# Optimization experiments

Hardware: AMD Instinct MI355X
Metric: run time of the kernel (lower is better)

The kernel has to match this reference:

```python
import jax, jax.numpy as jnp
import numpy as np

THRESHOLD = 0.2
NEG_POS_RATIO = 3
ALPHA = 1.0
B, M, P, C = 64, 50, 24564, 2


def cxcy_to_xy(c):
    return jnp.concatenate([c[..., :2] - c[..., 2:] / 2, c[..., :2] + c[..., 2:] / 2], axis=-1)


def xy_to_cxcy(x):
    return jnp.concatenate([(x[..., :2] + x[..., 2:]) / 2, x[..., 2:] - x[..., :2]], axis=-1)


def cxcy_to_gcxgcy(c, p):
    # SSD encoding: offsets scaled by 10, sizes (log) scaled by 5
    return jnp.concatenate([(c[..., :2] - p[..., :2]) / (p[..., 2:] / 10.0),
                            jnp.log(c[..., 2:] / p[..., 2:]) * 5.0], axis=-1)


def jaccard(a, b):
    # a: (M,4) xy boxes, b: (P,4) xy boxes -> (M,P) IoU
    lt = jnp.maximum(a[:, None, :2], b[None, :, :2])
    rb = jnp.minimum(a[:, None, 2:], b[None, :, 2:])
    inter = jnp.prod(jnp.clip(rb - lt, 0.0), axis=-1)
    area_a = jnp.prod(a[:, 2:] - a[:, :2], axis=-1)
    area_b = jnp.prod(b[:, 2:] - b[:, :2], axis=-1)
    return inter / (area_a[:, None] + area_b[None, :] - inter)


def setup_inputs() -> dict:
    key = jax.random.key(0)
    k1, k2, k3, k4, k5, k6 = jax.random.split(key, 6)
    predicted_locs = jax.random.normal(k1, (B, P, 4), dtype=jnp.float32)
    predicted_scores = jax.random.normal(k2, (B, P, C), dtype=jnp.float32)
    # valid GT corner boxes in [0,1]: x2>x1, y2>y1
    xy1 = jax.random.uniform(k3, (B, M, 2), minval=0.0, maxval=0.75)
    wh = jax.random.uniform(k4, (B, M, 2), minval=0.05, maxval=0.25)
    boxes = jnp.concatenate([xy1, xy1 + wh], axis=-1).astype(jnp.float32)
    # priors in cxcywh with positive sizes
    pc = jax.random.uniform(k5, (P, 2), minval=0.0, maxval=1.0)
    pwh = jax.random.uniform(k6, (P, 2), minval=0.02, maxval=0.3)
    priors_cxcy = jnp.concatenate([pc, pwh], axis=-1).astype(jnp.float32)
    return {"predicted_locs": predicted_locs, "predicted_scores": predicted_scores,
            "boxes": boxes, "priors_cxcy": priors_cxcy}


def reference(predicted_locs, predicted_scores, boxes, priors_cxcy):
    n_priors = priors_cxcy.shape[0]
    priors_xy = cxcy_to_xy(priors_cxcy)

    def assign(boxes_i):  # boxes_i: (M,4) xy
        overlap = jaccard(boxes_i, priors_xy)  # (M,P)
        overlap_for_each_prior = overlap.max(axis=0)        # (P,)
        object_for_each_prior = overlap.argmax(axis=0)      # (P,)
        prior_for_each_object = overlap.argmax(axis=1)      # (M,)
        # force each object's best prior to be assigned to that object
        object_for_each_prior = object_for_each_prior.at[prior_for_each_object].set(jnp.arange(boxes_i.shape[0]))
        overlap_for_each_prior = overlap_for_each_prior.at[prior_for_each_object].set(1.0)
        labels = jnp.where(overlap_for_each_prior < THRESHOLD, 0, 1).astype(jnp.int32)
        true_locs = cxcy_to_gcxgcy(xy_to_cxcy(boxes_i[object_for_each_prior]), priors_cxcy)
        return labels, true_locs

    true_classes, true_locs = jax.vmap(assign)(boxes)  # (B,P), (B,P,4)
    pos = true_classes != 0                            # (B,P)
    n_pos = pos.sum(axis=1)                            # (B,)
    total_pos = n_pos.sum().astype(jnp.float32)

    # L1Loss(mean) over the positive-prior coordinates
    loc_abs = jnp.abs(predicted_locs - true_locs)
    loc_loss = jnp.sum(loc_abs * pos[..., None]) / (total_pos * 4.0)

    # per-prior cross entropy
    logp = jax.nn.log_softmax(predicted_scores, axis=-1)
    conf_all = -jnp.take_along_axis(logp, true_classes[..., None].astype(jnp.int32), axis=-1)[..., 0]  # (B,P)
    conf_pos_sum = jnp.sum(conf_all * pos)

    # hard negative mining: zero positives, sort descending, take top 3*n_pos per image
    conf_neg = jnp.where(pos, 0.0, conf_all)
    conf_neg_sorted = -jnp.sort(-conf_neg, axis=1)
    ranks = jnp.arange(n_priors)[None, :]
    hard = ranks < (NEG_POS_RATIO * n_pos)[:, None]
    conf_hard_sum = jnp.sum(conf_neg_sorted * hard)

    conf_loss = (conf_hard_sum + conf_pos_sum) / total_pos
    return conf_loss + ALPHA * loc_loss
```

## Files before the change

### kernel.cpp

```cpp
#include <hip/hip_runtime.h>
#include <math.h>

#define BB 64
#define MM 50
#define PP 24564
#define NBLK 96
#define THRESH 0.2f
#define P4 (PP / 4)
#define SLACK 64u
#define NCH 24
#define WMARG 0.151f
#define RCPM 8u
#define NBINS 64
#define GBIN 8
#define BINBLK 24
#define SELCH 8
#define SCH4 ((P4 + SELCH - 1) / SELCH)
#define CAP PP

__device__ __forceinline__ float l1loc(float4 bxm, float4 pc, float4 pl) {
    float cx = (bxm.x + bxm.z) * 0.5f, cy = (bxm.y + bxm.w) * 0.5f;
    float w = bxm.z - bxm.x, h = bxm.w - bxm.y;
    float g0 = (cx - pc.x) / (pc.z * 0.1f);
    float g1 = (cy - pc.y) / (pc.w * 0.1f);
    float g2 = logf(w / pc.z) * 5.0f;
    float g3 = logf(h / pc.w) * 5.0f;
    return fabsf(pl.x - g0) + fabsf(pl.y - g1) + fabsf(pl.z - g2) + fabsf(pl.w - g3);
}

__global__ void k_init(int* __restrict__ ghist, int* __restrict__ ghist2,
                       int* __restrict__ gcur, unsigned long long* __restrict__ Lm) {
    int i = blockIdx.x * 256 + threadIdx.x;
    if (i < BB * 2048) ghist[i] = 0;
    if (i < BB * 1024) ghist2[i] = 0;
    if (i < BB) gcur[i] = 0;
    if (i < BB * MM) Lm[i] = 0x00000000FFFFFFFFull;
}

__global__ void k_bin_count(const float4* __restrict__ pr_cxcy, int* __restrict__ blkcnt) {
    __shared__ int h[NBINS];
    int tid = threadIdx.x;
    if (tid < NBINS) h[tid] = 0;
    __syncthreads();
    for (int p = blockIdx.x * 256 + tid; p < PP; p += BINBLK * 256) {
        float4 c = pr_cxcy[p];
        int bx = min(GBIN - 1, (int)(c.x * GBIN));
        int by = min(GBIN - 1, (int)(c.y * GBIN));
        atomicAdd(&h[by * GBIN + bx], 1);
    }
    __syncthreads();
    if (tid < NBINS) blkcnt[blockIdx.x * NBINS + tid] = h[tid];
}

__global__ void k_bin_scan(const int* __restrict__ blkcnt, int* __restrict__ blkbase) {
    __shared__ int s[NBINS];
    int tid = threadIdx.x;
    int cnt = 0;
    for (int k = 0; k < BINBLK; ++k) cnt += blkcnt[k * NBINS + tid];
    int v = cnt;
    s[tid] = v;
    __syncthreads();
    for (int off = 1; off < NBINS; off <<= 1) {
        int add = (tid >= off) ? s[tid - off] : 0;
        __syncthreads();
        v += add;
        s[tid] = v;
        __syncthreads();
    }
    int base = v - cnt;
    for (int k = 0; k < BINBLK; ++k) {
        blkbase[k * NBINS + tid] = base;
        base += blkcnt[k * NBINS + tid];
    }
}

__global__ void k_bin_scatter(const float4* __restrict__ pr_cxcy,
                              const int* __restrict__ blkbase,
                              float4* __restrict__ perm_pc,
                              int* __restrict__ perm_orig,
                              int* __restrict__ invperm) {
    __shared__ int cur[NBINS];
    int tid = threadIdx.x;
    if (tid < NBINS) cur[tid] = blkbase[blockIdx.x * NBINS + tid];
    __syncthreads();
    for (int p = blockIdx.x * 256 + tid; p < PP; p += BINBLK * 256) {
        float4 c = pr_cxcy[p];
        int bx = min(GBIN - 1, (int)(c.x * GBIN));
        int by = min(GBIN - 1, (int)(c.y * GBIN));
        int pos = atomicAdd(&cur[by * GBIN + bx], 1);
        perm_pc[pos] = c;
        perm_orig[pos] = p;
        invperm[p] = pos;
    }
}

__global__ void k_tilebb(const float4* __restrict__ perm_pc, float4* __restrict__ tilebox) {
    int t = blockIdx.x, tid = threadIdx.x;
    int slot = t * 256 + tid;
    float x1 = 1e30f, y1 = 1e30f, x2 = -1e30f, y2 = -1e30f;
    if (slot < PP) {
        float4 c = perm_pc[slot];
        x1 = c.x - c.z * 0.5f; y1 = c.y - c.w * 0.5f;
        x2 = c.x + c.z * 0.5f; y2 = c.y + c.w * 0.5f;
    }
    __shared__ float sx1[256], sy1[256], sx2[256], sy2[256];
    sx1[tid] = x1; sy1[tid] = y1; sx2[tid] = x2; sy2[tid] = y2;
    __syncthreads();
    for (int s = 128; s > 0; s >>= 1) {
        if (tid < s) {
            sx1[tid] = fminf(sx1[tid], sx1[tid + s]);
            sy1[tid] = fminf(sy1[tid], sy1[tid + s]);
            sx2[tid] = fmaxf(sx2[tid], sx2[tid + s]);
            sy2[tid] = fmaxf(sy2[tid], sy2[tid + s]);
        }
        __syncthreads();
    }
    if (tid == 0) tilebox[t] = make_float4(sx1[0], sy1[0], sx2[0], sy2[0]);
}

__global__ void k_main(const float4* __restrict__ boxes,
                       const float4* __restrict__ perm_pc,
                       const int* __restrict__ perm_orig,
                       const float4* __restrict__ tilebox,
                       const float4* __restrict__ plocs,
                       const float2* __restrict__ scores,
                       unsigned long long* __restrict__ Lm,
                       float* __restrict__ bestv,
                       int* __restrict__ bmv,
                       float* __restrict__ confneg,
                       int* __restrict__ ghist,
                       int* __restrict__ npos_part,
                       float* __restrict__ cpos_part,
                       float* __restrict__ loc_part) {
    int b = blockIdx.y;
    int slot = blockIdx.x * 256 + threadIdx.x;
    int tid = threadIdx.x;
    __shared__ float4 sbox[MM];
    __shared__ float sarea[MM];
    __shared__ unsigned long long smax[MM];
    __shared__ int shist[2048];
    __shared__ int si[256];
    __shared__ float s1[256], s2[256];
    __shared__ unsigned char slist[64];
    __shared__ int s_nc;
    for (int i = tid; i < 2048; i += 256) shist[i] = 0;
    if (tid < MM) {
        float4 bxt = boxes[b * MM + tid];
        sbox[tid] = bxt;
        sarea[tid] = (bxt.z - bxt.x) * (bxt.w - bxt.y);
        smax[tid] = 0ull;
    }
    __syncthreads();
    if (tid < 64) {
        float4 tb = tilebox[blockIdx.x];
        bool flag = false;
        if (tid < MM) {
            float4 bxm = sbox[tid];
            flag = !(bxm.x > tb.z || bxm.z < tb.x || bxm.y > tb.w || bxm.w < tb.y);
        }
        unsigned long long mask = __ballot(flag);
        if (flag) {
            int rank = __popcll(mask & ((1ull << tid) - 1));
            slist[rank] = (unsigned char)tid;
        }
        if (tid == 0) s_nc = __popcll(mask);
    }
    __syncthreads();

    int np = 0;
    float cpos = 0.0f, lloc = 0.0f;
    if (slot < PP) {
        float4 pc = perm_pc[slot];
        int orig = perm_orig[slot];
        float px1 = pc.x - pc.z * 0.5f, py1 = pc.y - pc.w * 0.5f;
        float px2 = pc.x + pc.z * 0.5f, py2 = pc.y + pc.w * 0.5f;
        float pa = (px2 - px1) * (py2 - py1);
        float binter = 0.0f, bdenom = 1.0f;
        int bm = 0;
        int nc = s_nc;
        for (int j = 0; j < nc; ++j) {
            int m = (int)slist[j];
            float4 bxm = sbox[m];
            float lx = fmaxf(bxm.x, px1), ly = fmaxf(bxm.y, py1);
            float rx = fminf(bxm.z, px2), ry = fminf(bxm.w, py2);
            float iw = fmaxf(rx - lx, 0.0f), ih = fmaxf(ry - ly, 0.0f);
            float inter = iw * ih;
            float den = sarea[m] + pa - inter;
            float l = inter * bdenom, r = binter * den;
            if (l > r) { binter = inter; bdenom = den; bm = m; }
        }
        float q = binter / bdenom;
        size_t sidx = (size_t)b * PP + slot;
        size_t oidx = (size_t)b * PP + orig;
        bestv[sidx] = q;
        bmv[sidx] = bm;
        unsigned long long key =
            ((unsigned long long)__float_as_uint(q) << 32) | (unsigned int)(~orig);
        atomicMax(&smax[bm], key);
        bool pos = (q >= THRESH);
        float2 sc = scores[oidx];
        float mx = fmaxf(sc.x, sc.y);
        float lse = mx + logf(expf(sc.x - mx) + expf(sc.y - mx));
        float conf = pos ? (lse - sc.y) : (lse - sc.x);
        float ck = pos ? 0.0f : conf;
        confneg[sidx] = ck;
        atomicAdd(&shist[__float_as_uint(ck) >> 20], 1);
        if (pos) {
            np = 1;
            cpos = conf;
            lloc = l1loc(sbox[bm], pc, plocs[oidx]);
        }
    }
    si[tid] = np; s1[tid] = cpos; s2[tid] = lloc;
    __syncthreads();
    for (int s = 128; s > 0; s >>= 1) {
        if (tid < s) {
            si[tid] += si[tid + s];
            s1[tid] += s1[tid + s];
            s2[tid] += s2[tid + s];
        }
        __syncthreads();
    }
    if (tid == 0) {
        int o = b * NBLK + blockIdx.x;
        npos_part[o] = si[0];
        cpos_part[o] = s1[0];
        loc_part[o] = s2[0];
    }
    if (tid < MM) {
        unsigned long long v = smax[tid];
        if (v) atomicMax(&Lm[b * MM + tid], v);
    }
    for (int i = tid; i < 2048; i += 256) {
        int c = shist[i];
        if (c) atomicAdd(&ghist[b * 2048 + i], c);
    }
}

__global__ void k_bpo3(const float4* __restrict__ boxes,
                       const float4* __restrict__ perm_pc,
                       const int* __restrict__ perm_orig,
                       const float* __restrict__ bestv,
                       unsigned long long* __restrict__ Lm) {
    int b = blockIdx.y, c = blockIdx.x, tid = threadIdx.x;
    __shared__ float4 sbox[MM];
    __shared__ float sarea[MM];
    __shared__ unsigned thr[MM];
    __shared__ unsigned thrs[MM];
    __shared__ unsigned char order[MM];
    __shared__ unsigned long long smax[MM];
    if (tid < MM) {
        float4 bxt = boxes[b * MM + tid];
        sbox[tid] = bxt;
        sarea[tid] = (bxt.z - bxt.x) * (bxt.w - bxt.y);
        unsigned long long L = Lm[b * MM + tid];
        smax[tid] = L;
        unsigned hi = (unsigned)(L >> 32);
        thr[tid] = (hi > SLACK) ? hi - SLACK : 0u;
    }
    __syncthreads();
    if (tid < MM) {
        unsigned tj = thr[tid];
        int rank = 0;
        for (int k = 0; k < MM; ++k) {
            unsigned tk = thr[k];
            if (tk < tj || (tk == tj && k < tid)) rank++;
        }
        order[rank] = (unsigned char)tid;
        thrs[rank] = tj;
    }
    __syncthreads();
    const unsigned* smax_hi = ((const unsigned*)smax) + 1;
    const float4* bv4 = (const float4*)(bestv + (size_t)b * PP);
    int i = c * 256 + tid;
    unsigned qb4[4] = {0u, 0u, 0u, 0u};
    int porig[4] = {0, 0, 0, 0};
    float4 pc4[4];
    float px1r[4], py1r[4], px2r[4], py2r[4], par[4];
    #pragma unroll
    for (int e = 0; e < 4; ++e) pc4[e] = make_float4(-10.0f, -10.0f, 0.0f, 0.0f);
    if (i < P4) {
        float4 qv = bv4[i];
        qb4[0] = __float_as_uint(qv.x); qb4[1] = __float_as_uint(qv.y);
        qb4[2] = __float_as_uint(qv.z); qb4[3] = __float_as_uint(qv.w);
        #pragma unroll
        for (int e = 0; e < 4; ++e) {
            pc4[e] = perm_pc[4 * i + e];
            porig[e] = perm_orig[4 * i + e];
        }
    }
    #pragma unroll
    for (int e = 0; e < 4; ++e) {
        px1r[e] = pc4[e].x - pc4[e].z * 0.5f;
        py1r[e] = pc4[e].y - pc4[e].w * 0.5f;
        px2r[e] = pc4[e].x + pc4[e].z * 0.5f;
        py2r[e] = pc4[e].y + pc4[e].w * 0.5f;
        par[e] = (px2r[e] - px1r[e]) * (py2r[e] - py1r[e]);
    }
    unsigned wqb = max(max(qb4[0], qb4[1]), max(qb4[2], qb4[3]));
    #pragma unroll
    for (int off = 32; off > 0; off >>= 1)
        wqb = max(wqb, (unsigned)__shfl_xor((int)wqb, off));

    unsigned thrv = thrs[0];
    int j = (int)order[0];
    float4 bxm = sbox[j];
    float am = sarea[j];
    unsigned hi = smax_hi[2 * j];
    for (int jj = 0; jj < MM; ++jj) {
        if (thrv > wqb) break;
        unsigned thrv_n = 0xFFFFFFFFu;
        int j_n = 0;
        float4 bxm_n = make_float4(0.0f, 0.0f, 0.0f, 0.0f);
        float am_n = 0.0f;
        unsigned hi_n = 0u;
        if (jj + 1 < MM) {
            thrv_n = thrs[jj + 1];
            j_n = (int)order[jj + 1];
            bxm_n = sbox[j_n];
            am_n = sarea[j_n];
            hi_n = smax_hi[2 * j_n];
        }
        unsigned long long hikey = ((unsigned long long)hi) << 32;
        #pragma unroll
        for (int e = 0; e < 4; ++e) {
            if (qb4[e] < thrv) continue;
            float4 pc = pc4[e];
            if (pc.x < bxm.x - WMARG || pc.x > bxm.z + WMARG ||
                pc.y < bxm.y - WMARG || pc.y > bxm.w + WMARG) continue;
            float lx = fmaxf(bxm.x, px1r[e]), ly = fmaxf(bxm.y, py1r[e]);
            float rx = fminf(bxm.z, px2r[e]), ry = fminf(bxm.w, py2r[e]);
            float iw = fmaxf(rx - lx, 0.0f), ih = fmaxf(ry - ly, 0.0f);
            float inter = iw * ih;
            float den = am + par[e] - inter;
            float qa = inter * __builtin_amdgcn_rcpf(den);
            if (__float_as_uint(qa) + RCPM < hi) continue;
            float q = inter / den;
            unsigned long long key =
                ((unsigned long long)__float_as_uint(q) << 32) |
                (unsigned int)(~porig[e]);
            if (key > hikey) atomicMax(&smax[j], key);
        }
        thrv = thrv_n; j = j_n; bxm = bxm_n; am = am_n; hi = hi_n;
    }
    __syncthreads();
    if (tid < MM) atomicMax(&Lm[b * MM + tid], smax[tid]);
}

__device__ __forceinline__ float block_sum(float v, float* fred, int tid) {
    fred[tid] = v;
    __syncthreads();
    for (int s = 128; s > 0; s >>= 1) {
        if (tid < s) fred[tid] += fred[tid + s];
        __syncthreads();
    }
    float r = fred[0];
    __syncthreads();
    return r;
}

template <int NB>
__device__ __forceinline__ void suffix_find(const int* __restrict__ h, int K, int tid,
                                            int* iscr, int* bcast, int slot) {
    const int c = NB / 256;
    const int base = tid * c;
    int tsum = 0;
    #pragma unroll
    for (int i = 0; i < c; ++i) tsum += h[base + i];
    iscr[tid] = tsum;
    __syncthreads();
    int val = tsum;
    for (int off = 1; off < 256; off <<= 1) {
        int other = (tid + off < 256) ? iscr[tid + off] : 0;
        __syncthreads();
        val += other;
        iscr[tid] = val;
        __syncthreads();
    }
    int acc = val - tsum;
    int best = -1, cg = 0;
    for (int i = base + c - 1; i >= base; --i) {
        int s = acc + h[i];
        if (s >= K) { best = i; cg = acc; break; }
        acc = s;
    }
    iscr[tid] = best;
    __syncthreads();
    for (int s2 = 128; s2 > 0; s2 >>= 1) {
        if (tid < s2) iscr[tid] = max(iscr[tid], iscr[tid + s2]);
        __syncthreads();
    }
    int gbest = iscr[0];
    __syncthreads();
    if (best == gbest && best >= 0) { bcast[slot] = gbest; bcast[slot + 1] = cg; }
    __syncthreads();
}

__global__ void k_selKF(const float4* __restrict__ boxes,
                        const float4* __restrict__ pr_cxcy,
                        const float4* __restrict__ plocs,
                        const float2* __restrict__ scores,
                        const unsigned long long* __restrict__ Lm,
                        const int* __restrict__ invperm,
                        const float* __restrict__ bestv,
                        const int* __restrict__ bmv,
                        float* __restrict__ confneg,
                        const int* __restrict__ ghist,
                        const int* __restrict__ npos_part,
                        int4* __restrict__ selp,
                        int* __restrict__ npfix,
                        float* __restrict__ cposfix,
                        float* __restrict__ llocfix) {
    int b = blockIdx.x, tid = threadIdx.x;
    __shared__ int h[2048];
    __shared__ int iscr[256];
    __shared__ int bcast[8];
    __shared__ int s_dnp;
    for (int i = tid; i < 2048; i += 256) h[i] = ghist[b * 2048 + i];
    __syncthreads();
    if (tid < 64) {
        int fp = -1;
        if (tid < MM) fp = (int)(~(unsigned)(Lm[b * MM + tid] & 0xFFFFFFFFull));
        bool active = (tid < MM);
        for (int m2 = 0; m2 < MM; ++m2) {
            int v = __shfl(fp, m2);
            if (m2 > tid && v == fp) active = false;
        }
        int dnp = 0;
        float dcp = 0.0f, dll = 0.0f;
        if (active) {
            int slot = invperm[fp];
            size_t sidx = (size_t)b * PP + slot;
            size_t oidx = (size_t)b * PP + fp;
            float bo = bestv[sidx];
            bool npold = (bo >= THRESH);
            float4 pc = pr_cxcy[fp];
            float4 pl = plocs[oidx];
            float llnew = l1loc(boxes[b * MM + tid], pc, pl);
            if (npold) {
                dll = llnew - l1loc(boxes[b * MM + bmv[sidx]], pc, pl);
            } else {
                float2 sc = scores[oidx];
                float mx = fmaxf(sc.x, sc.y);
                float lse = mx + logf(expf(sc.x - mx) + expf(sc.y - mx));
                dnp = 1;
                dcp = lse - sc.y;
                dll = llnew;
                float cold = confneg[sidx];
                atomicAdd(&h[(int)(__float_as_uint(cold) >> 20)], -1);
                atomicAdd(&h[0], 1);
                confneg[sidx] = 0.0f;
            }
        }
        #pragma unroll
        for (int off = 32; off > 0; off >>= 1) {
            dnp += __shfl_xor(dnp, off);
            dcp += __shfl_xor(dcp, off);
            dll += __shfl_xor(dll, off);
        }
        if (tid == 0) {
            s_dnp = dnp;
            npfix[b] = dnp; cposfix[b] = dcp; llocfix[b] = dll;
        }
    }
    __syncthreads();
    iscr[tid] = (tid < NBLK) ? npos_part[b * NBLK + tid] : 0;
    __syncthreads();
    for (int s = 128; s > 0; s >>= 1) {
        if (tid < s) iscr[tid] += iscr[tid + s];
        __syncthreads();
    }
    int npos = iscr[0] + s_dnp;
    __syncthreads();
    long long Kl = 3LL * npos;
    int K = (Kl > PP) ? PP : (int)Kl;
    if (K == 0) {
        if (tid == 0) selp[b] = make_int4(0, -1, 0, 0);
        return;
    }
    suffix_find<2048>(h, K, tid, iscr, bcast, 0);
    if (tid == 0) {
        int b1 = bcast[0];
        selp[b] = make_int4(K, b1, K - bcast[1], h[b1]);
    }
}

__global__ void k_selA(const float* __restrict__ confneg,
                       const int4* __restrict__ selp,
                       float* __restrict__ saP,
                       int* __restrict__ ghist2,
                       int* __restrict__ gcur,
                       float* __restrict__ gstore) {
    int b = blockIdx.y, c = blockIdx.x, tid = threadIdx.x;
    __shared__ float fred[256];
    __shared__ int h2[1024];
    __shared__ float sstore[SCH4 * 4];
    __shared__ int scnt, sbase;
    for (int i = tid; i < 1024; i += 256) h2[i] = 0;
    if (tid == 0) scnt = 0;
    __syncthreads();
    int4 sp = selp[b];
    int b1 = sp.y;
    float sa = 0.0f;
    if (b1 >= 0) {
        const float4* cn4 = (const float4*)(confneg + (size_t)b * PP);
        int i1 = min((c + 1) * SCH4, P4);
        for (int i = c * SCH4 + tid; i < i1; i += 256) {
            float4 q = cn4[i];
            float vv[4] = {q.x, q.y, q.z, q.w};
            #pragma unroll
            for (int j = 0; j < 4; ++j) {
                unsigned k = __float_as_uint(vv[j]);
                int t11 = (int)(k >> 20);
                if (t11 > b1) sa += vv[j];
                else if (t11 == b1) {
                    atomicAdd(&h2[(k >> 10) & 1023], 1);
                    int ix = atomicAdd(&scnt, 1);
                    sstore[ix] = vv[j];
                }
            }
        }
    }
    __syncthreads();
    if (tid == 0 && scnt > 0) sbase = atomicAdd(&gcur[b], scnt);
    __syncthreads();
    int n = scnt;
    for (int i = tid; i < n; i += 256)
        gstore[(size_t)b * CAP + sbase + i] = sstore[i];
    for (int i = tid; i < 1024; i += 256) {
        int v = h2[i];
        if (v) atomicAdd(&ghist2[b * 1024 + i], v);
    }
    float Sa = block_sum(sa, fred, tid);
    if (tid == 0) saP[b * SELCH + c] = Sa;
}

__global__ void k_selB(const int4* __restrict__ selp,
                       const float* __restrict__ saP,
                       const int* __restrict__ ghist2,
                       const float* __restrict__ gstore,
                       float* __restrict__ chard) {
    int b = blockIdx.x, tid = threadIdx.x;
    __shared__ int h[1024];
    __shared__ float fred[256];
    __shared__ int iscr[256];
    __shared__ int bcast[8];
    __shared__ float sSa;
    int4 sp = selp[b];
    if (sp.x == 0) {
        if (tid == 0) chard[b] = 0.0f;
        return;
    }
    int b1 = sp.y, K1 = sp.z, h1cnt = sp.w;
    if (tid == 0) {
        float s = 0.0f;
        for (int j = 0; j < SELCH; ++j) s += saP[b * SELCH + j];
        sSa = s;
    }
    for (int i = tid; i < 1024; i += 256) h[i] = ghist2[b * 1024 + i];
    __syncthreads();
    float Sa = sSa;
    suffix_find<1024>(h, K1, tid, iscr, bcast, 0);
    int b2 = bcast[0];
    int K2 = K1 - bcast[1];
    unsigned top21 = ((unsigned)b1 << 10) | (unsigned)b2;
    __syncthreads();

    const float* gs = gstore + (size_t)b * CAP;
    for (int i = tid; i < 1024; i += 256) h[i] = 0;
    __syncthreads();
    float sb = 0.0f;
    for (int i = tid; i < h1cnt; i += 256) {
        float v = gs[i];
        unsigned k = __float_as_uint(v);
        int n10 = (int)((k >> 10) & 1023);
        if (n10 > b2) sb += v;
        else if (n10 == b2) atomicAdd(&h[k & 1023], 1);
    }
    float Sb = block_sum(sb, fred, tid);
    suffix_find<1024>(h, K2, tid, iscr, bcast, 2);
    int b3 = bcast[2];
    int K3 = K2 - bcast[3];
    float sc = 0.0f;
    for (int i = tid; i < h1cnt; i += 256) {
        float v = gs[i];
        unsigned k = __float_as_uint(v);
        if ((k >> 10) == top21 && (k & 1023) > (unsigned)b3) sc += v;
    }
    float Sc = block_sum(sc, fred, tid);
    if (tid == 0) {
        unsigned kstar = (top21 << 10) | (unsigned)b3;
        chard[b] = Sa + Sb + Sc + (float)K3 * __uint_as_float(kstar);
    }
}

__global__ void k_final(const int* __restrict__ npos_part,
                        const float* __restrict__ cpos_part,
                        const float* __restrict__ loc_part,
                        const float* __restrict__ chard,
                        const int* __restrict__ npfix,
                        const float* __restrict__ cposfix,
                        const float* __restrict__ llocfix,
                        float* __restrict__ out) {
    __shared__ int si[256];
    __shared__ float s1[256], s2[256], s3[256];
    int tn = 0; float tc = 0.0f, tl = 0.0f, th = 0.0f;
    for (int i = threadIdx.x; i < BB * NBLK; i += 256) {
        tn += npos_part[i];
        tc += cpos_part[i];
        tl += loc_part[i];
    }
    if (threadIdx.x < BB) {
        th = chard[threadIdx.x];
        tn += npfix[threadIdx.x];
        tc += cposfix[threadIdx.x];
        tl += llocfix[threadIdx.x];
    }
    si[threadIdx.x] = tn; s1[threadIdx.x] = tc; s2[threadIdx.x] = tl; s3[threadIdx.x] = th;
    __syncthreads();
    for (int s = 128; s > 0; s >>= 1) {
        if (threadIdx.x < s) {
            si[threadIdx.x] += si[threadIdx.x + s];
            s1[threadIdx.x] += s1[threadIdx.x + s];
            s2[threadIdx.x] += s2[threadIdx.x + s];
            s3[threadIdx.x] += s3[threadIdx.x + s];
        }
        __syncthreads();
    }
    if (threadIdx.x == 0) {
        float tp = (float)si[0];
        out[0] = (s3[0] + s1[0]) / tp + s2[0] / (tp * 4.0f);
    }
}

extern "C" void kernel_launch(void* const* d_in, const int* in_sizes, int n_in,
                              void* d_out, int out_size, void* d_ws, size_t ws_size,
                              hipStream_t stream) {
    const float4* plocs   = (const float4*)d_in[0];
    const float2* scores  = (const float2*)d_in[1];
    const float4* boxes   = (const float4*)d_in[2];
    const float4* priors  = (const float4*)d_in[3];
    float* out = (float*)d_out;

    char* ws = (char*)d_ws;
    size_t off = 0;
    auto alloc = [&](size_t bytes) -> void* {
        void* p = ws + off;
        off += (bytes + 255) & ~(size_t)255;
        return p;
    };
    float*              confneg  = (float*) alloc((size_t)BB * PP * 4);
    float*              bestv    = (float*) alloc((size_t)BB * PP * 4);
    int*                bmv      = (int*)   alloc((size_t)BB * PP * 4);
    int*                ghist    = (int*)   alloc((size_t)BB * 2048 * 4);
    int*                ghist2   = (int*)   alloc((size_t)BB * 1024 * 4);
    unsigned long long* Lm       = (unsigned long long*)alloc((size_t)BB * MM * 8);
    float4*             perm_pc  = (float4*)alloc((size_t)(NBLK * 256) * 16);
    int*                perm_orig= (int*)   alloc((size_t)(NBLK * 256) * 4);
    int*                invperm  = (int*)   alloc((size_t)PP * 4);
    float4*             tilebox  = (float4*)alloc((size_t)NBLK * 16);
    int*                blkcnt   = (int*)   alloc((size_t)BINBLK * NBINS * 4);
    int*                blkbase  = (int*)   alloc((size_t)BINBLK * NBINS * 4);
    int*                npos_p   = (int*)   alloc((size_t)BB * NBLK * 4);
    float*              cpos_p   = (float*) alloc((size_t)BB * NBLK * 4);
    float*              loc_p    = (float*) alloc((size_t)BB * NBLK * 4);
    float*              chard    = (float*) alloc((size_t)BB * 4);
    int*                npfix    = (int*)   alloc((size_t)BB * 4);
    float*              cposfix  = (float*) alloc((size_t)BB * 4);
    float*              llocfix  = (float*) alloc((size_t)BB * 4);
    int4*               selp     = (int4*)  alloc((size_t)BB * 16);
    float*              saP      = (float*) alloc((size_t)BB * SELCH * 4);
    int*                gcur     = (int*)   alloc((size_t)BB * 4);
    float*              gstore   = (float*) alloc((size_t)BB * CAP * 4);
    (void)ws_size; (void)in_sizes; (void)n_in; (void)out_size;

    k_init<<<512, 256, 0, stream>>>(ghist, ghist2, gcur, Lm);
    k_bin_count<<<BINBLK, 256, 0, stream>>>(priors, blkcnt);
    k_bin_scan<<<1, 64, 0, stream>>>(blkcnt, blkbase);
    k_bin_scatter<<<BINBLK, 256, 0, stream>>>(priors, blkbase, perm_pc, perm_orig, invperm);
    k_tilebb<<<NBLK, 256, 0, stream>>>(perm_pc, tilebox);
    k_main<<<dim3(NBLK, BB), 256, 0, stream>>>(boxes, perm_pc, perm_orig, tilebox,
                                               plocs, scores, Lm, bestv, bmv,
                                               confneg, ghist, npos_p, cpos_p, loc_p);
    k_bpo3<<<dim3(NCH, BB), 256, 0, stream>>>(boxes, perm_pc, perm_orig, bestv, Lm);
    k_selKF<<<BB, 256, 0, stream>>>(boxes, priors, plocs, scores, Lm, invperm,
                                    bestv, bmv, confneg, ghist, npos_p, selp,
                                    npfix, cposfix, llocfix);
    k_selA<<<dim3(SELCH, BB), 256, 0, stream>>>(confneg, selp, saP, ghist2, gcur, gstore);
    k_selB<<<BB, 256, 0, stream>>>(selp, saP, ghist2, gstore, chard);
    k_final<<<1, 256, 0, stream>>>(npos_p, cpos_p, loc_p, chard,
                                   npfix, cposfix, llocfix, out);
}
```

Measured before the change: 141.4 us.

## Rebalance radix-select histograms to 8/12/11 bits and add chunk bbox culling in bpo3

The first-level histogram of confidence bits for hard-negative top-k selection now uses the top 8 bits (256 bins) instead of 11, with second and third levels widened to 12 and 11 bits. This makes the main kernel's shared histogram and global atomic flush much smaller, at the cost of a larger second-level histogram in selA/selB and more candidates in the tie bucket. Separately, k_bpo3 builds a bounding box over its four prior tiles and skips whole GT boxes whose margin window misses it, avoiding per-prior IoU checks.

```diff
diff --git a/kernel.cpp b/kernel.cpp
--- a/kernel.cpp
+++ b/kernel.cpp
@@ -31,8 +31,8 @@
 __global__ void k_init(int* __restrict__ ghist, int* __restrict__ ghist2,
                        int* __restrict__ gcur, unsigned long long* __restrict__ Lm) {
     int i = blockIdx.x * 256 + threadIdx.x;
-    if (i < BB * 2048) ghist[i] = 0;
-    if (i < BB * 1024) ghist2[i] = 0;
+    if (i < BB * 256) ghist[i] = 0;
+    if (i < BB * 4096) ghist2[i] = 0;
     if (i < BB) gcur[i] = 0;
     if (i < BB * MM) Lm[i] = 0x00000000FFFFFFFFull;
 }
@@ -138,12 +138,12 @@
     __shared__ float4 sbox[MM];
     __shared__ float sarea[MM];
     __shared__ unsigned long long smax[MM];
-    __shared__ int shist[2048];
+    __shared__ int shist[256];
     __shared__ int si[256];
     __shared__ float s1[256], s2[256];
     __shared__ unsigned char slist[64];
     __shared__ int s_nc;
-    for (int i = tid; i < 2048; i += 256) shist[i] = 0;
+    shist[tid] = 0;
     if (tid < MM) {
         float4 bxt = boxes[b * MM + tid];
         sbox[tid] = bxt;
@@ -204,7 +204,7 @@
         float conf = pos ? (lse - sc.y) : (lse - sc.x);
         float ck = pos ? 0.0f : conf;
         confneg[sidx] = ck;
-        atomicAdd(&shist[__float_as_uint(ck) >> 20], 1);
+        atomicAdd(&shist[__float_as_uint(ck) >> 23], 1);
         if (pos) {
             np = 1;
             cpos = conf;
@@ -231,15 +231,16 @@
         unsigned long long v = smax[tid];
         if (v) atomicMax(&Lm[b * MM + tid], v);
     }
-    for (int i = tid; i < 2048; i += 256) {
-        int c = shist[i];
-        if (c) atomicAdd(&ghist[b * 2048 + i], c);
+    {
+        int c = shist[tid];
+        if (c) atomicAdd(&ghist[b * 256 + tid], c);
     }
 }
 
 __global__ void k_bpo3(const float4* __restrict__ boxes,
                        const float4* __restrict__ perm_pc,
                        const int* __restrict__ perm_orig,
+                       const float4* __restrict__ tilebox,
                        const float* __restrict__ bestv,
                        unsigned long long* __restrict__ Lm) {
     int b = blockIdx.y, c = blockIdx.x, tid = threadIdx.x;
@@ -270,6 +271,13 @@
         thrs[rank] = tj;
     }
     __syncthreads();
+    float cbx1 = 1e30f, cby1 = 1e30f, cbx2 = -1e30f, cby2 = -1e30f;
+    #pragma unroll
+    for (int t = 0; t < 4; ++t) {
+        float4 tb = tilebox[c * 4 + t];
+        cbx1 = fminf(cbx1, tb.x); cby1 = fminf(cby1, tb.y);
+        cbx2 = fmaxf(cbx2, tb.z); cby2 = fmaxf(cby2, tb.w);
+    }
     const unsigned* smax_hi = ((const unsigned*)smax) + 1;
     const float4* bv4 = (const float4*)(bestv + (size_t)b * PP);
     int i = c * 256 + tid;
@@ -321,25 +329,29 @@
             am_n = sarea[j_n];
             hi_n = smax_hi[2 * j_n];
         }
-        unsigned long long hikey = ((unsigned long long)hi) << 32;
-        #pragma unroll
-        for (int e = 0; e < 4; ++e) {
-            if (qb4[e] < thrv) continue;
-            float4 pc = pc4[e];
-            if (pc.x < bxm.x - WMARG || pc.x > bxm.z + WMARG ||
-                pc.y < bxm.y - WMARG || pc.y > bxm.w + WMARG) continue;
-            float lx = fmaxf(bxm.x, px1r[e]), ly = fmaxf(bxm.y, py1r[e]);
-            float rx = fminf(bxm.z, px2r[e]), ry = fminf(bxm.w, py2r[e]);
-            float iw = fmaxf(rx - lx, 0.0f), ih = fmaxf(ry - ly, 0.0f);
-            float inter = iw * ih;
-            float den = am + par[e] - inter;
-            float qa = inter * __builtin_amdgcn_rcpf(den);
-            if (__float_as_uint(qa) + RCPM < hi) continue;
-            float q = inter / den;
-            unsigned long long key =
-                ((unsigned long long)__float_as_uint(q) << 32) |
-                (unsigned int)(~porig[e]);
-            if (key > hikey) atomicMax(&smax[j], key);
+        bool skip = (bxm.x - WMARG > cbx2 || bxm.z + WMARG < cbx1 ||
+                     bxm.y - WMARG > cby2 || bxm.w + WMARG < cby1);
+        if (!skip) {
+            unsigned long long hikey = ((unsigned long long)hi) << 32;
+            #pragma unroll
+            for (int e = 0; e < 4; ++e) {
+                if (qb4[e] < thrv) continue;
+                float4 pc = pc4[e];
+                if (pc.x < bxm.x - WMARG || pc.x > bxm.z + WMARG ||
+                    pc.y < bxm.y - WMARG || pc.y > bxm.w + WMARG) continue;
+                float lx = fmaxf(bxm.x, px1r[e]), ly = fmaxf(bxm.y, py1r[e]);
+                float rx = fminf(bxm.z, px2r[e]), ry = fminf(bxm.w, py2r[e]);
+                float iw = fmaxf(rx - lx, 0.0f), ih = fmaxf(ry - ly, 0.0f);
+                float inter = iw * ih;
+                float den = am + par[e] - inter;
+                float qa = inter * __builtin_amdgcn_rcpf(den);
+                if (__float_as_uint(qa) + RCPM < hi) continue;
+                float q = inter / den;
+                unsigned long long key =
+                    ((unsigned long long)__float_as_uint(q) << 32) |
+                    (unsigned int)(~porig[e]);
+                if (key > hikey) atomicMax(&smax[j], key);
+            }
         }
         thrv = thrv_n; j = j_n; bxm = bxm_n; am = am_n; hi = hi_n;
     }
@@ -412,11 +424,11 @@
                         float* __restrict__ cposfix,
                         float* __restrict__ llocfix) {
     int b = blockIdx.x, tid = threadIdx.x;
-    __shared__ int h[2048];
+    __shared__ int h[256];
     __shared__ int iscr[256];
     __shared__ int bcast[8];
     __shared__ int s_dnp;
-    for (int i = tid; i < 2048; i += 256) h[i] = ghist[b * 2048 + i];
+    h[tid] = ghist[b * 256 + tid];
     __syncthreads();
     if (tid < 64) {
         int fp = -1;
@@ -447,7 +459,7 @@
                 dcp = lse - sc.y;
                 dll = llnew;
                 float cold = confneg[sidx];
-                atomicAdd(&h[(int)(__float_as_uint(cold) >> 20)], -1);
+                atomicAdd(&h[(int)(__float_as_uint(cold) >> 23)], -1);
                 atomicAdd(&h[0], 1);
                 confneg[sidx] = 0.0f;
             }
@@ -478,7 +490,7 @@
         if (tid == 0) selp[b] = make_int4(0, -1, 0, 0);
         return;
     }
-    suffix_find<2048>(h, K, tid, iscr, bcast, 0);
+    suffix_find<256>(h, K, tid, iscr, bcast, 0);
     if (tid == 0) {
         int b1 = bcast[0];
         selp[b] = make_int4(K, b1, K - bcast[1], h[b1]);
@@ -493,10 +505,10 @@
                        float* __restrict__ gstore) {
     int b = blockIdx.y, c = blockIdx.x, tid = threadIdx.x;
     __shared__ float fred[256];
-    __shared__ int h2[1024];
+    __shared__ int h2[4096];
     __shared__ float sstore[SCH4 * 4];
     __shared__ int scnt, sbase;
-    for (int i = tid; i < 1024; i += 256) h2[i] = 0;
+    for (int i = tid; i < 4096; i += 256) h2[i] = 0;
     if (tid == 0) scnt = 0;
     __syncthreads();
     int4 sp = selp[b];
@@ -511,10 +523,10 @@
             #pragma unroll
             for (int j = 0; j < 4; ++j) {
                 unsigned k = __float_as_uint(vv[j]);
-                int t11 = (int)(k >> 20);
-                if (t11 > b1) sa += vv[j];
-                else if (t11 == b1) {
-                    atomicAdd(&h2[(k >> 10) & 1023], 1);
+                int t8 = (int)(k >> 23);
+                if (t8 > b1) sa += vv[j];
+                else if (t8 == b1) {
+                    atomicAdd(&h2[(k >> 11) & 4095], 1);
                     int ix = atomicAdd(&scnt, 1);
                     sstore[ix] = vv[j];
                 }
@@ -527,9 +539,9 @@
     int n = scnt;
     for (int i = tid; i < n; i += 256)
         gstore[(size_t)b * CAP + sbase + i] = sstore[i];
-    for (int i = tid; i < 1024; i += 256) {
+    for (int i = tid; i < 4096; i += 256) {
         int v = h2[i];
-        if (v) atomicAdd(&ghist2[b * 1024 + i], v);
+        if (v) atomicAdd(&ghist2[b * 4096 + i], v);
     }
     float Sa = block_sum(sa, fred, tid);
     if (tid == 0) saP[b * SELCH + c] = Sa;
@@ -541,7 +553,7 @@
                        const float* __restrict__ gstore,
                        float* __restrict__ chard) {
     int b = blockIdx.x, tid = threadIdx.x;
-    __shared__ int h[1024];
+    __shared__ int h[4096];
     __shared__ float fred[256];
     __shared__ int iscr[256];
     __shared__ int bcast[8];
@@ -557,39 +569,38 @@
         for (int j = 0; j < SELCH; ++j) s += saP[b * SELCH + j];
         sSa = s;
     }
-    for (int i = tid; i < 1024; i += 256) h[i] = ghist2[b * 1024 + i];
+    for (int i = tid; i < 4096; i += 256) h[i] = ghist2[b * 4096 + i];
     __syncthreads();
     float Sa = sSa;
-    suffix_find<1024>(h, K1, tid, iscr, bcast, 0);
+    suffix_find<4096>(h, K1, tid, iscr, bcast, 0);
     int b2 = bcast[0];
     int K2 = K1 - bcast[1];
-    unsigned top21 = ((unsigned)b1 << 10) | (unsigned)b2;
     __syncthreads();
 
     const float* gs = gstore + (size_t)b * CAP;
-    for (int i = tid; i < 1024; i += 256) h[i] = 0;
+    for (int i = tid; i < 2048; i += 256) h[i] = 0;
     __syncthreads();
     float sb = 0.0f;
     for (int i = tid; i < h1cnt; i += 256) {
         float v = gs[i];
         unsigned k = __float_as_uint(v);
-        int n10 = (int)((k >> 10) & 1023);
-        if (n10 > b2) sb += v;
-        else if (n10 == b2) atomicAdd(&h[k & 1023], 1);
+        int n12 = (int)((k >> 11) & 4095);
+        if (n12 > b2) sb += v;
+        else if (n12 == b2) atomicAdd(&h[k & 2047], 1);
     }
     float Sb = block_sum(sb, fred, tid);
-    suffix_find<1024>(h, K2, tid, iscr, bcast, 2);
+    suffix_find<2048>(h, K2, tid, iscr, bcast, 2);
     int b3 = bcast[2];
     int K3 = K2 - bcast[3];
     float sc = 0.0f;
     for (int i = tid; i < h1cnt; i += 256) {
         float v = gs[i];
         unsigned k = __float_as_uint(v);
-        if ((k >> 10) == top21 && (k & 1023) > (unsigned)b3) sc += v;
+        if ((int)((k >> 11) & 4095) == b2 && (k & 2047) > (unsigned)b3) sc += v;
     }
     float Sc = block_sum(sc, fred, tid);
     if (tid == 0) {
-        unsigned kstar = (top21 << 10) | (unsigned)b3;
+        unsigned kstar = ((unsigned)b1 << 23) | ((unsigned)b2 << 11) | (unsigned)b3;
         chard[b] = Sa + Sb + Sc + (float)K3 * __uint_as_float(kstar);
     }
 }
@@ -652,8 +663,8 @@
     float*              confneg  = (float*) alloc((size_t)BB * PP * 4);
     float*              bestv    = (float*) alloc((size_t)BB * PP * 4);
     int*                bmv      = (int*)   alloc((size_t)BB * PP * 4);
-    int*                ghist    = (int*)   alloc((size_t)BB * 2048 * 4);
-    int*                ghist2   = (int*)   alloc((size_t)BB * 1024 * 4);
+    int*                ghist    = (int*)   alloc((size_t)BB * 256 * 4);
+    int*                ghist2   = (int*)   alloc((size_t)BB * 4096 * 4);
     unsigned long long* Lm       = (unsigned long long*)alloc((size_t)BB * MM * 8);
     float4*             perm_pc  = (float4*)alloc((size_t)(NBLK * 256) * 16);
     int*                perm_orig= (int*)   alloc((size_t)(NBLK * 256) * 4);
@@ -674,7 +685,7 @@
     float*              gstore   = (float*) alloc((size_t)BB * CAP * 4);
     (void)ws_size; (void)in_sizes; (void)n_in; (void)out_size;
 
-    k_init<<<512, 256, 0, stream>>>(ghist, ghist2, gcur, Lm);
+    k_init<<<1024, 256, 0, stream>>>(ghist, ghist2, gcur, Lm);
     k_bin_count<<<BINBLK, 256, 0, stream>>>(priors, blkcnt);
     k_bin_scan<<<1, 64, 0, stream>>>(blkcnt, blkbase);
     k_bin_scatter<<<BINBLK, 256, 0, stream>>>(priors, blkbase, perm_pc, perm_orig, invperm);
@@ -682,7 +693,7 @@
     k_main<<<dim3(NBLK, BB), 256, 0, stream>>>(boxes, perm_pc, perm_orig, tilebox,
                                                plocs, scores, Lm, bestv, bmv,
                                                confneg, ghist, npos_p, cpos_p, loc_p);
-    k_bpo3<<<dim3(NCH, BB), 256, 0, stream>>>(boxes, perm_pc, perm_orig, bestv, Lm);
+    k_bpo3<<<dim3(NCH, BB), 256, 0, stream>>>(boxes, perm_pc, perm_orig, tilebox, bestv, Lm);
     k_selKF<<<BB, 256, 0, stream>>>(boxes, priors, plocs, scores, Lm, invperm,
                                     bestv, bmv, confneg, ghist, npos_p, selp,
                                     npfix, cposfix, llocfix);
```

After: 143.1 us. No clear change (+1.2%).
